# Kernel tuning notes

Hardware: AMD Instinct MI355X
Metric: run time of the kernel (lower is better)

The kernel has to match this reference:

```python
import jax, jax.numpy as jnp
import numpy as np
from jax import lax

T, B, DX, H, DZ = 512, 64, 128, 256, 64
W_SCALE = 0.05


def setup_inputs() -> dict:
    key = jax.random.key(0)
    ks = jax.random.split(key, 16)
    r = lambda k, shape, s=W_SCALE: jax.random.normal(k, shape, dtype=jnp.float32) * s
    return {
        "X": jax.random.normal(ks[0], (T, B, DX), dtype=jnp.float32),
        "Wih_f": r(ks[1], (H, DX)), "Whh_f": r(ks[2], (H, H)),
        "bih_f": r(ks[3], (H,)), "bhh_f": r(ks[4], (H,)),
        "Wih_b": r(ks[5], (H, DX)), "Whh_b": r(ks[6], (H, H)),
        "bih_b": r(ks[7], (H,)), "bhh_b": r(ks[8], (H,)),
        "Wt": r(ks[9], (H, DZ)), "bt": r(ks[10], (H,)),
        "Wmu": r(ks[11], (DZ, H)), "bmu": r(ks[12], (DZ,)),
        "Wsig": r(ks[13], (DZ, H)), "bsig": r(ks[14], (DZ,)),
        "eps": jax.random.normal(ks[15], (T, B, DZ), dtype=jnp.float32),
    }


def _rnn_dir(X, Wih, Whh, bih, bhh):
    # Elman RNN (tanh): h_t = tanh(x_t Wih^T + bih + h_{t-1} Whh^T + bhh)
    xproj = jnp.einsum('tbd,hd->tbh', X, Wih) + bih + bhh  # big GEMM hoisted out of scan

    def step(h, xp):
        h = jnp.tanh(xp + h @ Whh.T)
        return h, h

    h0 = jnp.zeros((X.shape[1], Whh.shape[0]), dtype=X.dtype)
    _, hs = lax.scan(step, h0, xproj)
    return hs  # [T,B,H]


def reference(X, Wih_f, Whh_f, bih_f, bhh_f, Wih_b, Whh_b, bih_b, bhh_b,
              Wt, bt, Wmu, bmu, Wsig, bsig, eps):
    h_left = _rnn_dir(X, Wih_f, Whh_f, bih_f, bhh_f)
    h_right = _rnn_dir(X[::-1], Wih_b, Whh_b, bih_b, bhh_b)[::-1]

    def step(z_prev, inputs):
        hl, hr, eps_t = inputs
        tmp = jnp.tanh(z_prev @ Wt.T + bt)           # transition_net
        h_t = (tmp + hl + hr) * (1.0 / 3.0)
        mu = h_t @ Wmu.T + bmu
        std = jax.nn.softplus(h_t @ Wsig.T + bsig)
        z = mu + std * eps_t                         # reparameterization
        return z, (z, mu, std)

    z0 = jnp.zeros((X.shape[1], Wt.shape[1]), dtype=X.dtype)
    _, (z, mu, std) = lax.scan(step, z0, (h_left, h_right, eps))
    # stack outputs {z_post, mu_post, std_post} into one array [3,T,B,DZ]
    return jnp.stack([z, mu, std])
```

## Files before the change

kernel.cpp:

```cpp
#include <hip/hip_runtime.h>

#define TT 512
#define BB 64
#define DXX 128
#define HH 256
#define DZZ 64

typedef __attribute__((ext_vector_type(8))) short short8;
typedef __attribute__((ext_vector_type(4))) float f32x4;

#define DEV static __device__ __forceinline__
#define MFMA(a,b,c) __builtin_amdgcn_mfma_f32_16x16x32_bf16((a),(b),(c),0,0,0)

DEV unsigned short f2bf(float f){
  unsigned u = __builtin_bit_cast(unsigned, f);
  u += 0x7FFFu + ((u >> 16) & 1u);
  return (unsigned short)(u >> 16);
}
DEV unsigned pack2(float lo, float hi){
  return (unsigned)f2bf(lo) | ((unsigned)f2bf(hi) << 16);
}
DEV float bfLO(unsigned u){ return __builtin_bit_cast(float, u << 16); }
DEV float bfHI(unsigned u){ return __builtin_bit_cast(float, u & 0xffff0000u); }
DEV float ftanh(float x){
  float a = fabsf(x);
  float e = __expf(-2.f * a);
  float r = __builtin_amdgcn_rcpf(1.f + e);
  float t = (1.f - e) * r;
  return copysignf(t, x);
}
DEV float fsoftplus(float x){
  float e = __expf(fminf(x, 20.f));
  float s = __logf(1.f + e);
  return (x > 20.f) ? x : s;
}
DEV void barrier_l(){
  asm volatile("s_waitcnt lgkmcnt(0)\n\ts_barrier" ::: "memory");
}


__global__ __launch_bounds__(256, 2) void phaseA(
    const float* __restrict__ X,
    const float* __restrict__ WihF, const float* __restrict__ bihF, const float* __restrict__ bhhF,
    const float* __restrict__ WihB, const float* __restrict__ bihB, const float* __restrict__ bhhB,
    unsigned short* __restrict__ xpF)
{
  const int bid = blockIdx.x;
  const int d = bid >> 9, s = bid & 511;
  const int ts = d ? (TT - 1 - s) : s;
  const float* W  = d ? WihB : WihF;
  const float* bi = d ? bihB : bihF;
  const float* bh = d ? bhhB : bhhF;

  const int tid = threadIdx.x, q = tid >> 6, l = tid & 63;
  const int l15 = l & 15, l4 = l >> 4;

  short8 wf[4][4];
  f32x4 bias[4];
  #pragma unroll
  for (int ni = 0; ni < 4; ++ni){
    int n = 64*q + 16*ni + l15;
    #pragma unroll
    for (int ks = 0; ks < 4; ++ks){
      const float* p = W + (size_t)n * DXX + ks*32 + l4*8;
      short8 v;
      #pragma unroll
      for (int i = 0; i < 8; ++i) v[i] = (short)f2bf(p[i]);
      wf[ni][ks] = v;
    }
    int n0 = 64*q + 16*ni + 4*l4;
    float4 b1 = *(const float4*)(bi + n0);
    float4 b2 = *(const float4*)(bh + n0);
    bias[ni][0]=b1.x+b2.x; bias[ni][1]=b1.y+b2.y; bias[ni][2]=b1.z+b2.z; bias[ni][3]=b1.w+b2.w;
  }

  #pragma unroll
  for (int bq = 0; bq < 4; ++bq){
    const float* xr = X + ((size_t)ts * 64 + 16*bq + l15) * DXX;
    short8 xf[4];
    #pragma unroll
    for (int ks = 0; ks < 4; ++ks){
      const float* p = xr + ks*32 + l4*8;
      short8 v;
      #pragma unroll
      for (int i = 0; i < 8; ++i) v[i] = (short)f2bf(p[i]);
      xf[ks] = v;
    }

    f32x4 acc[4];
    #pragma unroll
    for (int ni = 0; ni < 4; ++ni) acc[ni] = MFMA(wf[ni][0], xf[0], bias[ni]);
    #pragma unroll
    for (int ks = 1; ks < 4; ++ks)
      #pragma unroll
      for (int ni = 0; ni < 4; ++ni)
        acc[ni] = MFMA(wf[ni][ks], xf[ks], acc[ni]);

    unsigned wd[8];
    #pragma unroll
    for (int ni = 0; ni < 4; ++ni){
      wd[ni*2]   = pack2(acc[ni][0], acc[ni][1]);
      wd[ni*2+1] = pack2(acc[ni][2], acc[ni][3]);
    }
    unsigned short* dst = xpF + ((((size_t)d*TT + s)*4 + bq)*4 + q)*1024 + (size_t)l*16;
    uint4 o0 = {wd[0], wd[1], wd[2], wd[3]};
    uint4 o1 = {wd[4], wd[5], wd[6], wd[7]};
    ((uint4*)dst)[0] = o0;
    ((uint4*)dst)[1] = o1;
  }
}

__global__ __launch_bounds__(256, 1) void phaseB(
    const float* __restrict__ WhhF, const float* __restrict__ WhhB,
    const unsigned short* __restrict__ xpF, unsigned short* __restrict__ hF)
{
  const int dir = blockIdx.x >> 2, bq = blockIdx.x & 3;
  const float* Whh = dir ? WhhB : WhhF;
  const int tid = threadIdx.x, q = tid >> 6, l = tid & 63;
  const int l15 = l & 15, l4 = l >> 4;
  const int swz = (l15 & 7) << 3;
  const int rbase = l15 * 256;

  __shared__ __attribute__((aligned(16))) unsigned short hbuf[2][4096];

  short8 wf[4][8];
  #pragma unroll
  for (int ni = 0; ni < 4; ++ni){
    int n = 64*q + 16*ni + l15;
    #pragma unroll
    for (int ks = 0; ks < 8; ++ks){
      const float* p = Whh + (size_t)n * HH + ks*32 + l4*8;
      short8 v;
      #pragma unroll
      for (int i = 0; i < 8; ++i) v[i] = (short)f2bf(p[i]);
      wf[ni][ks] = v;
    }
  }
  for (int i = tid; i < 2048; i += 256) ((unsigned*)hbuf[0])[i] = 0u;

  const size_t strideS = 16384;
  const size_t laneOff = (size_t)bq*4096 + (size_t)q*1024 + (size_t)l*16;
  const unsigned short* xpP = xpF + (size_t)dir*TT*strideS + laneOff;
  unsigned short* hD = hF + (size_t)dir*TT*strideS + laneOff;

  uint4 xqA0, xqA1, xqB0, xqB1;
  { const uint4* p = (const uint4*)xpP;             xqA0 = p[0]; xqA1 = p[1]; }
  { const uint4* p = (const uint4*)(xpP + strideS); xqB0 = p[0]; xqB1 = p[1]; }

  barrier_l();

  auto bstep = [&](int s, uint4& XQ0, uint4& XQ1,
                   const unsigned short* RD, unsigned short* WR){
    short8 b[8];
    #pragma unroll
    for (int ks = 0; ks < 8; ++ks)
      b[ks] = *(const short8*)(RD + ((rbase + ks*32 + l4*8) ^ swz));
    f32x4 accE[4], accO[4];
    {
      unsigned W8[8] = {XQ0.x, XQ0.y, XQ0.z, XQ0.w, XQ1.x, XQ1.y, XQ1.z, XQ1.w};
      #pragma unroll
      for (int ni = 0; ni < 4; ++ni){
        accE[ni][0] = bfLO(W8[ni*2]);   accE[ni][1] = bfHI(W8[ni*2]);
        accE[ni][2] = bfLO(W8[ni*2+1]); accE[ni][3] = bfHI(W8[ni*2+1]);
        accO[ni][0] = 0.f; accO[ni][1] = 0.f; accO[ni][2] = 0.f; accO[ni][3] = 0.f;
      }
    }
    {
      int sn = (s + 2 < TT) ? s + 2 : TT - 1;
      const uint4* src = (const uint4*)(xpP + (size_t)sn * strideS);
      XQ0 = src[0]; XQ1 = src[1];
    }
    #pragma unroll
    for (int ks = 0; ks < 8; ks += 2){
      #pragma unroll
      for (int ni = 0; ni < 4; ++ni){
        accE[ni] = MFMA(wf[ni][ks],   b[ks],   accE[ni]);
        accO[ni] = MFMA(wf[ni][ks+1], b[ks+1], accO[ni]);
      }
    }
    unsigned wd[8];
    #pragma unroll
    for (int ni = 0; ni < 4; ++ni){
      float t0 = ftanh(accE[ni][0] + accO[ni][0]);
      float t1 = ftanh(accE[ni][1] + accO[ni][1]);
      float t2 = ftanh(accE[ni][2] + accO[ni][2]);
      float t3 = ftanh(accE[ni][3] + accO[ni][3]);
      unsigned lo = pack2(t0, t1), hi = pack2(t2, t3);
      wd[ni*2] = lo; wd[ni*2+1] = hi;
      int ea = rbase + ((64*q + 16*ni + 4*l4) ^ swz);
      uint2 v; v.x = lo; v.y = hi;
      *(uint2*)(WR + ea) = v;
    }
    {
      size_t off = (size_t)(dir ? (TT - 1 - s) : s) * strideS;
      uint4 o0 = {wd[0], wd[1], wd[2], wd[3]};
      uint4 o1 = {wd[4], wd[5], wd[6], wd[7]};
      *(uint4*)(hD + off)     = o0;
      *(uint4*)(hD + off + 8) = o1;
    }
    barrier_l();
  };

  for (int s = 0; s < TT; s += 2){
    bstep(s,     xqA0, xqA1, hbuf[0], hbuf[1]);
    bstep(s + 1, xqB0, xqB1, hbuf[1], hbuf[0]);
  }
}

__global__ __launch_bounds__(256, 1) void phaseC(
    const float* __restrict__ Wt,  const float* __restrict__ bt,
    const float* __restrict__ Wmu, const float* __restrict__ bmu,
    const float* __restrict__ Wsig,const float* __restrict__ bsig,
    const float* __restrict__ eps, const unsigned short* __restrict__ hF,
    float* __restrict__ out)
{
  const int bq = blockIdx.x;
  const int tid = threadIdx.x, q = tid >> 6, l = tid & 63;
  const int l15 = l & 15, l4 = l >> 4;
  const int swz = (l15 & 7) << 3;
  const int rbase = l15 * 256;
  const int zrbase = l15 * 64;

  __shared__ __attribute__((aligned(16))) unsigned short zbuf[1024];
  __shared__ __attribute__((aligned(16))) unsigned short hbuf[4096];

  short8 wtf[4][2]; f32x4 btb[4];
  #pragma unroll
  for (int ni = 0; ni < 4; ++ni){
    int n = 64*q + 16*ni + l15;
    #pragma unroll
    for (int ks = 0; ks < 2; ++ks){
      const float* p = Wt + (size_t)n * DZZ + ks*32 + l4*8;
      short8 v;
      #pragma unroll
      for (int i = 0; i < 8; ++i) v[i] = (short)f2bf(p[i]);
      wtf[ni][ks] = v;
    }
    float4 b4 = *(const float4*)(bt + 64*q + 16*ni + 4*l4);
    btb[ni][0]=b4.x; btb[ni][1]=b4.y; btb[ni][2]=b4.z; btb[ni][3]=b4.w;
  }
  short8 wm[8], wsg[8];
  {
    int r = 16*q + l15;
    #pragma unroll
    for (int ks = 0; ks < 8; ++ks){
      const float* pm = Wmu  + (size_t)r * HH + ks*32 + l4*8;
      const float* ps = Wsig + (size_t)r * HH + ks*32 + l4*8;
      short8 vm, vs;
      #pragma unroll
      for (int i = 0; i < 8; ++i){ vm[i] = (short)f2bf(pm[i]); vs[i] = (short)f2bf(ps[i]); }
      wm[ks] = vm; wsg[ks] = vs;
    }
  }
  f32x4 bm4, bs4;
  {
    float4 a = *(const float4*)(bmu  + 16*q + 4*l4);
    float4 b = *(const float4*)(bsig + 16*q + 4*l4);
    bm4[0]=a.x; bm4[1]=a.y; bm4[2]=a.z; bm4[3]=a.w;
    bs4[0]=b.x; bs4[1]=b.y; bs4[2]=b.z; bs4[3]=b.w;
  }
  for (int i = tid; i < 512; i += 256) ((unsigned*)zbuf)[i] = 0u;

  const size_t strideS = 16384;
  const size_t laneOff = (size_t)bq*4096 + (size_t)q*1024 + (size_t)l*16;
  const unsigned short* hLp = hF + laneOff;
  const unsigned short* hRp = hLp + (size_t)TT * strideS;
  const float* eP = eps + ((size_t)(16*bq + l15)) * 64 + 16*q + 4*l4;

  uint4 hlA0, hlA1, hrA0, hrA1, hlB0, hlB1, hrB0, hrB1;
  f32x4 efA, efB;
  {
    const uint4* sl = (const uint4*)hLp;              hlA0 = sl[0]; hlA1 = sl[1];
    const uint4* sr = (const uint4*)hRp;              hrA0 = sr[0]; hrA1 = sr[1];
    const uint4* tl = (const uint4*)(hLp + strideS);  hlB0 = tl[0]; hlB1 = tl[1];
    const uint4* tr = (const uint4*)(hRp + strideS);  hrB0 = tr[0]; hrB1 = tr[1];
    float4 e0 = *(const float4*)eP;
    float4 e1 = *(const float4*)(eP + 4096);
    efA[0]=e0.x; efA[1]=e0.y; efA[2]=e0.z; efA[3]=e0.w;
    efB[0]=e1.x; efB[1]=e1.y; efB[2]=e1.z; efB[3]=e1.w;
  }
  const size_t TBZ = (size_t)TT * 64 * 64;
  const f32x4 zero4 = {0.f, 0.f, 0.f, 0.f};
  barrier_l();

  auto cstep = [&](int t, uint4& HL0, uint4& HL1, uint4& HR0, uint4& HR1, f32x4& EF){
    short8 zb0 = *(const short8*)(zbuf + ((zrbase +  0 + l4*8) ^ swz));
    short8 zb1 = *(const short8*)(zbuf + ((zrbase + 32 + l4*8) ^ swz));
    f32x4 at[4];
    #pragma unroll
    for (int ni = 0; ni < 4; ++ni) at[ni] = MFMA(wtf[ni][0], zb0, btb[ni]);
    #pragma unroll
    for (int ni = 0; ni < 4; ++ni) at[ni] = MFMA(wtf[ni][1], zb1, at[ni]);
    {
      unsigned HLw[8] = {HL0.x, HL0.y, HL0.z, HL0.w, HL1.x, HL1.y, HL1.z, HL1.w};
      unsigned HRw[8] = {HR0.x, HR0.y, HR0.z, HR0.w, HR1.x, HR1.y, HR1.z, HR1.w};
      #pragma unroll
      for (int ni = 0; ni < 4; ++ni){
        unsigned wl0 = HLw[ni*2], wl1 = HLw[ni*2+1];
        unsigned wr0 = HRw[ni*2], wr1 = HRw[ni*2+1];
        float h0 = (ftanh(at[ni][0]) + bfLO(wl0) + bfLO(wr0)) * (1.f/3.f);
        float h1 = (ftanh(at[ni][1]) + bfHI(wl0) + bfHI(wr0)) * (1.f/3.f);
        float h2 = (ftanh(at[ni][2]) + bfLO(wl1) + bfLO(wr1)) * (1.f/3.f);
        float h3 = (ftanh(at[ni][3]) + bfHI(wl1) + bfHI(wr1)) * (1.f/3.f);
        int ea = rbase + ((64*q + 16*ni + 4*l4) ^ swz);
        uint2 v; v.x = pack2(h0, h1); v.y = pack2(h2, h3);
        *(uint2*)(hbuf + ea) = v;
      }
    }
    {
      int tn = (t + 2 < TT) ? t + 2 : TT - 1;
      const uint4* sl = (const uint4*)(hLp + (size_t)tn*strideS);
      const uint4* sr = (const uint4*)(hRp + (size_t)tn*strideS);
      HL0 = sl[0]; HL1 = sl[1]; HR0 = sr[0]; HR1 = sr[1];
    }
    barrier_l();

    short8 hb[8];
    #pragma unroll
    for (int ks = 0; ks < 8; ++ks)
      hb[ks] = *(const short8*)(hbuf + ((rbase + ks*32 + l4*8) ^ swz));
    f32x4 am0 = MFMA(wm[0],  hb[0], bm4);
    f32x4 as0 = MFMA(wsg[0], hb[0], bs4);
    f32x4 am1 = MFMA(wm[4],  hb[4], zero4);
    f32x4 as1 = MFMA(wsg[4], hb[4], zero4);
    #pragma unroll
    for (int ks = 1; ks < 4; ++ks){
      am0 = MFMA(wm[ks],    hb[ks],   am0);
      as0 = MFMA(wsg[ks],   hb[ks],   as0);
      am1 = MFMA(wm[ks+4],  hb[ks+4], am1);
      as1 = MFMA(wsg[ks+4], hb[ks+4], as1);
    }
    f32x4 mu = am0 + am1;
    f32x4 sg = as0 + as1;
    f32x4 dz, dsp;
    #pragma unroll
    for (int reg = 0; reg < 4; ++reg){
      float sp = fsoftplus(sg[reg]);
      dz[reg] = __builtin_fmaf(sp, EF[reg], mu[reg]);
      dsp[reg] = sp;
    }
    {
      int zea = zrbase + ((16*q + 4*l4) ^ swz);
      uint2 v; v.x = pack2(dz[0], dz[1]); v.y = pack2(dz[2], dz[3]);
      *(uint2*)(zbuf + zea) = v;
    }
    {
      int tn = (t + 2 < TT) ? t + 2 : TT - 1;
      float4 e4 = *(const float4*)(eP + (size_t)tn*4096);
      EF[0]=e4.x; EF[1]=e4.y; EF[2]=e4.z; EF[3]=e4.w;
    }
    {
      size_t ob = ((size_t)t*64 + 16*bq + l15)*64 + 16*q + 4*l4;
      *(float4*)(out + ob)         = *(float4*)&dz;
      *(float4*)(out + TBZ + ob)   = *(float4*)&mu;
      *(float4*)(out + 2*TBZ + ob) = *(float4*)&dsp;
    }
    barrier_l();
  };

  for (int t = 0; t < TT; t += 2){
    cstep(t,     hlA0, hlA1, hrA0, hrA1, efA);
    cstep(t + 1, hlB0, hlB1, hrB0, hrB1, efB);
  }
}

extern "C" void kernel_launch(void* const* d_in, const int* in_sizes, int n_in,
                              void* d_out, int out_size, void* d_ws, size_t ws_size,
                              hipStream_t stream)
{
  const float* X      = (const float*)d_in[0];
  const float* Wih_f  = (const float*)d_in[1];
  const float* Whh_f  = (const float*)d_in[2];
  const float* bih_f  = (const float*)d_in[3];
  const float* bhh_f  = (const float*)d_in[4];
  const float* Wih_b  = (const float*)d_in[5];
  const float* Whh_b  = (const float*)d_in[6];
  const float* bih_b  = (const float*)d_in[7];
  const float* bhh_b  = (const float*)d_in[8];
  const float* Wt     = (const float*)d_in[9];
  const float* bt     = (const float*)d_in[10];
  const float* Wmu    = (const float*)d_in[11];
  const float* bmu    = (const float*)d_in[12];
  const float* Wsig   = (const float*)d_in[13];
  const float* bsig   = (const float*)d_in[14];
  const float* eps    = (const float*)d_in[15];

  unsigned short* xpF = (unsigned short*)d_ws;
  unsigned short* hF  = xpF + (size_t)2 * TT * 16384;

  phaseA<<<dim3(1024), dim3(256), 0, stream>>>(X, Wih_f, bih_f, bhh_f, Wih_b, bih_b, bhh_b, xpF);
  phaseB<<<dim3(8), dim3(256), 0, stream>>>(Whh_f, Whh_b, xpF, hF);
  phaseC<<<dim3(4), dim3(256), 0, stream>>>(Wt, bt, Wmu, bmu, Wsig, bsig, eps, hF, (float*)d_out);
}
```

Baseline: 1.132 ms.

## Hoist hl+hr projections out of latent scan and halve recurrence block width

The latent scan's mu/sigma projections are linear in h_t, so the hl+hr contribution is precomputed for all timesteps in a new fully parallel kernel and written to workspace. The sequential scan then only multiplies the tanh(transition) term by Wmu/Wsig, with the 1/3 factor folded into the weights. Both sequential kernels now use two waves per block instead of four, each wave owning twice as many output columns. This is meant to cut barrier cost and per-step latency on the serial critical path. The trade-offs are an extra kernel launch, extra workspace traffic, and more register pressure per wave.

```diff
diff --git a/kernel.cpp b/kernel.cpp
--- a/kernel.cpp
+++ b/kernel.cpp
@@ -1,7 +1,6 @@
 #include <hip/hip_runtime.h>
 
 #define TT 512
-#define BB 64
 #define DXX 128
 #define HH 256
 #define DZZ 64
@@ -86,7 +85,6 @@
       for (int i = 0; i < 8; ++i) v[i] = (short)f2bf(p[i]);
       xf[ks] = v;
     }
-
     f32x4 acc[4];
     #pragma unroll
     for (int ni = 0; ni < 4; ++ni) acc[ni] = MFMA(wf[ni][0], xf[0], bias[ni]);
@@ -110,135 +108,127 @@
   }
 }
 
-__global__ __launch_bounds__(256, 1) void phaseB(
+__global__ __launch_bounds__(128, 1) void phaseB(
     const float* __restrict__ WhhF, const float* __restrict__ WhhB,
     const unsigned short* __restrict__ xpF, unsigned short* __restrict__ hF)
 {
   const int dir = blockIdx.x >> 2, bq = blockIdx.x & 3;
   const float* Whh = dir ? WhhB : WhhF;
+  const int tid = threadIdx.x, qc = tid >> 6, l = tid & 63;
+  const int l15 = l & 15, l4 = l >> 4;
+  const int swz = (l15 & 7) << 3;
+  const int rbase = l15 * 256;
+
+  __shared__ __attribute__((aligned(16))) unsigned short hbuf[2][4096];
+
+  short8 wf[8][8];
+  #pragma unroll
+  for (int ni = 0; ni < 8; ++ni){
+    int n = 128*qc + 16*ni + l15;
+    #pragma unroll
+    for (int ks = 0; ks < 8; ++ks){
+      const float* p = Whh + (size_t)n * HH + ks*32 + l4*8;
+      short8 v;
+      #pragma unroll
+      for (int i = 0; i < 8; ++i) v[i] = (short)f2bf(p[i]);
+      wf[ni][ks] = v;
+    }
+  }
+  for (int i = tid; i < 2048; i += 128) ((unsigned*)hbuf[0])[i] = 0u;
+
+  const size_t strideS = 16384;
+  const size_t base = (size_t)dir*TT*strideS + (size_t)bq*4096 + (size_t)l*16;
+  const unsigned short* xpP = xpF + base;
+  unsigned short* hD = hF + base;
+
+  uint4 xA[4], xB[4];
+  #pragma unroll
+  for (int hi = 0; hi < 2; ++hi)
+    #pragma unroll
+    for (int pt = 0; pt < 2; ++pt){
+      xA[hi*2+pt] = *(const uint4*)(xpP + (size_t)(2*qc+hi)*1024 + pt*8);
+      xB[hi*2+pt] = *(const uint4*)(xpP + strideS + (size_t)(2*qc+hi)*1024 + pt*8);
+    }
+  barrier_l();
+
+  auto bstep = [&](int s, uint4 (&X)[4]){
+    f32x4 acc[8];
+    #pragma unroll
+    for (int ni = 0; ni < 8; ++ni){
+      int hi = ni >> 2, no = ni & 3;
+      uint4 u = X[hi*2 + (no >> 1)];
+      unsigned w0 = (no & 1) ? u.z : u.x;
+      unsigned w1 = (no & 1) ? u.w : u.y;
+      acc[ni][0] = bfLO(w0); acc[ni][1] = bfHI(w0);
+      acc[ni][2] = bfLO(w1); acc[ni][3] = bfHI(w1);
+    }
+    {
+      int sn = (s + 2 < TT) ? s + 2 : TT - 1;
+      #pragma unroll
+      for (int hi = 0; hi < 2; ++hi)
+        #pragma unroll
+        for (int pt = 0; pt < 2; ++pt)
+          X[hi*2+pt] = *(const uint4*)(xpP + (size_t)sn*strideS + (size_t)(2*qc+hi)*1024 + pt*8);
+    }
+    const unsigned short* RD = hbuf[s & 1];
+    unsigned short* WR = hbuf[(s & 1) ^ 1];
+    #pragma unroll
+    for (int ksc = 0; ksc < 8; ksc += 4){
+      short8 b[4];
+      #pragma unroll
+      for (int k2 = 0; k2 < 4; ++k2)
+        b[k2] = *(const short8*)(RD + ((rbase + (ksc+k2)*32 + l4*8) ^ swz));
+      #pragma unroll
+      for (int k2 = 0; k2 < 4; ++k2)
+        #pragma unroll
+        for (int ni = 0; ni < 8; ++ni)
+          acc[ni] = MFMA(wf[ni][ksc+k2], b[k2], acc[ni]);
+    }
+    unsigned wd[16];
+    #pragma unroll
+    for (int ni = 0; ni < 8; ++ni){
+      float t0 = ftanh(acc[ni][0]), t1 = ftanh(acc[ni][1]);
+      float t2 = ftanh(acc[ni][2]), t3 = ftanh(acc[ni][3]);
+      unsigned lo = pack2(t0, t1), hi2 = pack2(t2, t3);
+      wd[ni*2] = lo; wd[ni*2+1] = hi2;
+      int ea = rbase + ((128*qc + 16*ni + 4*l4) ^ swz);
+      uint2 v; v.x = lo; v.y = hi2;
+      *(uint2*)(WR + ea) = v;
+    }
+    {
+      size_t off = (size_t)(dir ? (TT - 1 - s) : s) * strideS;
+      #pragma unroll
+      for (int hi = 0; hi < 2; ++hi){
+        unsigned short* dst = hD + off + (size_t)(2*qc+hi)*1024;
+        uint4 o0 = {wd[hi*8+0], wd[hi*8+1], wd[hi*8+2], wd[hi*8+3]};
+        uint4 o1 = {wd[hi*8+4], wd[hi*8+5], wd[hi*8+6], wd[hi*8+7]};
+        *(uint4*)dst       = o0;
+        *(uint4*)(dst + 8) = o1;
+      }
+    }
+    barrier_l();
+  };
+
+  for (int s = 0; s < TT; s += 2){
+    bstep(s,     xA);
+    bstep(s + 1, xB);
+  }
+}
+
+__global__ __launch_bounds__(256, 2) void phaseP(
+    const float* __restrict__ Wmu, const float* __restrict__ bmu,
+    const float* __restrict__ Wsig,const float* __restrict__ bsig,
+    const unsigned short* __restrict__ hF, float* __restrict__ MS)
+{
+  const int bid = blockIdx.x;
+  const int t = bid >> 2, bq = bid & 3;
   const int tid = threadIdx.x, q = tid >> 6, l = tid & 63;
   const int l15 = l & 15, l4 = l >> 4;
   const int swz = (l15 & 7) << 3;
   const int rbase = l15 * 256;
 
-  __shared__ __attribute__((aligned(16))) unsigned short hbuf[2][4096];
-
-  short8 wf[4][8];
-  #pragma unroll
-  for (int ni = 0; ni < 4; ++ni){
-    int n = 64*q + 16*ni + l15;
-    #pragma unroll
-    for (int ks = 0; ks < 8; ++ks){
-      const float* p = Whh + (size_t)n * HH + ks*32 + l4*8;
-      short8 v;
-      #pragma unroll
-      for (int i = 0; i < 8; ++i) v[i] = (short)f2bf(p[i]);
-      wf[ni][ks] = v;
-    }
-  }
-  for (int i = tid; i < 2048; i += 256) ((unsigned*)hbuf[0])[i] = 0u;
-
-  const size_t strideS = 16384;
-  const size_t laneOff = (size_t)bq*4096 + (size_t)q*1024 + (size_t)l*16;
-  const unsigned short* xpP = xpF + (size_t)dir*TT*strideS + laneOff;
-  unsigned short* hD = hF + (size_t)dir*TT*strideS + laneOff;
-
-  uint4 xqA0, xqA1, xqB0, xqB1;
-  { const uint4* p = (const uint4*)xpP;             xqA0 = p[0]; xqA1 = p[1]; }
-  { const uint4* p = (const uint4*)(xpP + strideS); xqB0 = p[0]; xqB1 = p[1]; }
-
-  barrier_l();
-
-  auto bstep = [&](int s, uint4& XQ0, uint4& XQ1,
-                   const unsigned short* RD, unsigned short* WR){
-    short8 b[8];
-    #pragma unroll
-    for (int ks = 0; ks < 8; ++ks)
-      b[ks] = *(const short8*)(RD + ((rbase + ks*32 + l4*8) ^ swz));
-    f32x4 accE[4], accO[4];
-    {
-      unsigned W8[8] = {XQ0.x, XQ0.y, XQ0.z, XQ0.w, XQ1.x, XQ1.y, XQ1.z, XQ1.w};
-      #pragma unroll
-      for (int ni = 0; ni < 4; ++ni){
-        accE[ni][0] = bfLO(W8[ni*2]);   accE[ni][1] = bfHI(W8[ni*2]);
-        accE[ni][2] = bfLO(W8[ni*2+1]); accE[ni][3] = bfHI(W8[ni*2+1]);
-        accO[ni][0] = 0.f; accO[ni][1] = 0.f; accO[ni][2] = 0.f; accO[ni][3] = 0.f;
-      }
-    }
-    {
-      int sn = (s + 2 < TT) ? s + 2 : TT - 1;
-      const uint4* src = (const uint4*)(xpP + (size_t)sn * strideS);
-      XQ0 = src[0]; XQ1 = src[1];
-    }
-    #pragma unroll
-    for (int ks = 0; ks < 8; ks += 2){
-      #pragma unroll
-      for (int ni = 0; ni < 4; ++ni){
-        accE[ni] = MFMA(wf[ni][ks],   b[ks],   accE[ni]);
-        accO[ni] = MFMA(wf[ni][ks+1], b[ks+1], accO[ni]);
-      }
-    }
-    unsigned wd[8];
-    #pragma unroll
-    for (int ni = 0; ni < 4; ++ni){
-      float t0 = ftanh(accE[ni][0] + accO[ni][0]);
-      float t1 = ftanh(accE[ni][1] + accO[ni][1]);
-      float t2 = ftanh(accE[ni][2] + accO[ni][2]);
-      float t3 = ftanh(accE[ni][3] + accO[ni][3]);
-      unsigned lo = pack2(t0, t1), hi = pack2(t2, t3);
-      wd[ni*2] = lo; wd[ni*2+1] = hi;
-      int ea = rbase + ((64*q + 16*ni + 4*l4) ^ swz);
-      uint2 v; v.x = lo; v.y = hi;
-      *(uint2*)(WR + ea) = v;
-    }
-    {
-      size_t off = (size_t)(dir ? (TT - 1 - s) : s) * strideS;
-      uint4 o0 = {wd[0], wd[1], wd[2], wd[3]};
-      uint4 o1 = {wd[4], wd[5], wd[6], wd[7]};
-      *(uint4*)(hD + off)     = o0;
-      *(uint4*)(hD + off + 8) = o1;
-    }
-    barrier_l();
-  };
-
-  for (int s = 0; s < TT; s += 2){
-    bstep(s,     xqA0, xqA1, hbuf[0], hbuf[1]);
-    bstep(s + 1, xqB0, xqB1, hbuf[1], hbuf[0]);
-  }
-}
-
-__global__ __launch_bounds__(256, 1) void phaseC(
-    const float* __restrict__ Wt,  const float* __restrict__ bt,
-    const float* __restrict__ Wmu, const float* __restrict__ bmu,
-    const float* __restrict__ Wsig,const float* __restrict__ bsig,
-    const float* __restrict__ eps, const unsigned short* __restrict__ hF,
-    float* __restrict__ out)
-{
-  const int bq = blockIdx.x;
-  const int tid = threadIdx.x, q = tid >> 6, l = tid & 63;
-  const int l15 = l & 15, l4 = l >> 4;
-  const int swz = (l15 & 7) << 3;
-  const int rbase = l15 * 256;
-  const int zrbase = l15 * 64;
-
-  __shared__ __attribute__((aligned(16))) unsigned short zbuf[1024];
   __shared__ __attribute__((aligned(16))) unsigned short hbuf[4096];
 
-  short8 wtf[4][2]; f32x4 btb[4];
-  #pragma unroll
-  for (int ni = 0; ni < 4; ++ni){
-    int n = 64*q + 16*ni + l15;
-    #pragma unroll
-    for (int ks = 0; ks < 2; ++ks){
-      const float* p = Wt + (size_t)n * DZZ + ks*32 + l4*8;
-      short8 v;
-      #pragma unroll
-      for (int i = 0; i < 8; ++i) v[i] = (short)f2bf(p[i]);
-      wtf[ni][ks] = v;
-    }
-    float4 b4 = *(const float4*)(bt + 64*q + 16*ni + 4*l4);
-    btb[ni][0]=b4.x; btb[ni][1]=b4.y; btb[ni][2]=b4.z; btb[ni][3]=b4.w;
-  }
   short8 wm[8], wsg[8];
   {
     int r = 16*q + l15;
@@ -248,7 +238,10 @@
       const float* ps = Wsig + (size_t)r * HH + ks*32 + l4*8;
       short8 vm, vs;
       #pragma unroll
-      for (int i = 0; i < 8; ++i){ vm[i] = (short)f2bf(pm[i]); vs[i] = (short)f2bf(ps[i]); }
+      for (int i = 0; i < 8; ++i){
+        vm[i] = (short)f2bf(pm[i] * (1.f/3.f));
+        vs[i] = (short)f2bf(ps[i] * (1.f/3.f));
+      }
       wm[ks] = vm; wsg[ks] = vs;
     }
   }
@@ -259,108 +252,198 @@
     bm4[0]=a.x; bm4[1]=a.y; bm4[2]=a.z; bm4[3]=a.w;
     bs4[0]=b.x; bs4[1]=b.y; bs4[2]=b.z; bs4[3]=b.w;
   }
-  for (int i = tid; i < 512; i += 256) ((unsigned*)zbuf)[i] = 0u;
 
   const size_t strideS = 16384;
   const size_t laneOff = (size_t)bq*4096 + (size_t)q*1024 + (size_t)l*16;
-  const unsigned short* hLp = hF + laneOff;
-  const unsigned short* hRp = hLp + (size_t)TT * strideS;
-  const float* eP = eps + ((size_t)(16*bq + l15)) * 64 + 16*q + 4*l4;
-
-  uint4 hlA0, hlA1, hrA0, hrA1, hlB0, hlB1, hrB0, hrB1;
-  f32x4 efA, efB;
+  const unsigned short* hl = hF + (size_t)t*strideS + laneOff;
+  const unsigned short* hr = hl + (size_t)TT*strideS;
   {
-    const uint4* sl = (const uint4*)hLp;              hlA0 = sl[0]; hlA1 = sl[1];
-    const uint4* sr = (const uint4*)hRp;              hrA0 = sr[0]; hrA1 = sr[1];
-    const uint4* tl = (const uint4*)(hLp + strideS);  hlB0 = tl[0]; hlB1 = tl[1];
-    const uint4* tr = (const uint4*)(hRp + strideS);  hrB0 = tr[0]; hrB1 = tr[1];
-    float4 e0 = *(const float4*)eP;
-    float4 e1 = *(const float4*)(eP + 4096);
-    efA[0]=e0.x; efA[1]=e0.y; efA[2]=e0.z; efA[3]=e0.w;
-    efB[0]=e1.x; efB[1]=e1.y; efB[2]=e1.z; efB[3]=e1.w;
-  }
+    uint4 a0 = ((const uint4*)hl)[0], a1 = ((const uint4*)hl)[1];
+    uint4 b0 = ((const uint4*)hr)[0], b1 = ((const uint4*)hr)[1];
+    unsigned HL[8] = {a0.x,a0.y,a0.z,a0.w,a1.x,a1.y,a1.z,a1.w};
+    unsigned HR[8] = {b0.x,b0.y,b0.z,b0.w,b1.x,b1.y,b1.z,b1.w};
+    #pragma unroll
+    for (int ni = 0; ni < 4; ++ni){
+      float h0 = bfLO(HL[ni*2])   + bfLO(HR[ni*2]);
+      float h1 = bfHI(HL[ni*2])   + bfHI(HR[ni*2]);
+      float h2 = bfLO(HL[ni*2+1]) + bfLO(HR[ni*2+1]);
+      float h3 = bfHI(HL[ni*2+1]) + bfHI(HR[ni*2+1]);
+      int ea = rbase + ((64*q + 16*ni + 4*l4) ^ swz);
+      uint2 v; v.x = pack2(h0, h1); v.y = pack2(h2, h3);
+      *(uint2*)(hbuf + ea) = v;
+    }
+  }
+  __syncthreads();
+
+  short8 hb[8];
+  #pragma unroll
+  for (int ks = 0; ks < 8; ++ks)
+    hb[ks] = *(const short8*)(hbuf + ((rbase + ks*32 + l4*8) ^ swz));
+  const f32x4 zero4 = {0.f,0.f,0.f,0.f};
+  f32x4 am0 = MFMA(wm[0],  hb[0], bm4);
+  f32x4 as0 = MFMA(wsg[0], hb[0], bs4);
+  f32x4 am1 = MFMA(wm[4],  hb[4], zero4);
+  f32x4 as1 = MFMA(wsg[4], hb[4], zero4);
+  #pragma unroll
+  for (int ks = 1; ks < 4; ++ks){
+    am0 = MFMA(wm[ks],    hb[ks],   am0);
+    as0 = MFMA(wsg[ks],   hb[ks],   as0);
+    am1 = MFMA(wm[ks+4],  hb[ks+4], am1);
+    as1 = MFMA(wsg[ks+4], hb[ks+4], as1);
+  }
+  f32x4 mu = am0 + am1;
+  f32x4 sg = as0 + as1;
+  float* dst = MS + ((((size_t)t*4 + bq)*4 + q)*64 + (size_t)l)*8;
+  *(float4*)dst       = *(float4*)&mu;
+  *(float4*)(dst + 4) = *(float4*)&sg;
+}
+
+__global__ __launch_bounds__(128, 1) void phaseC(
+    const float* __restrict__ Wt,  const float* __restrict__ bt,
+    const float* __restrict__ Wmu, const float* __restrict__ Wsig,
+    const float* __restrict__ eps, const float* __restrict__ MS,
+    float* __restrict__ out)
+{
+  const int bq = blockIdx.x;
+  const int tid = threadIdx.x, qc = tid >> 6, l = tid & 63;
+  const int l15 = l & 15, l4 = l >> 4;
+  const int swz = (l15 & 7) << 3;
+  const int rbase = l15 * 256;
+  const int zrbase = l15 * 64;
+
+  __shared__ __attribute__((aligned(16))) unsigned short zbuf[1024];
+  __shared__ __attribute__((aligned(16))) unsigned short ubuf[4096];
+
+  short8 wtf[8][2]; f32x4 btb[8];
+  #pragma unroll
+  for (int ni = 0; ni < 8; ++ni){
+    int n = 128*qc + 16*ni + l15;
+    #pragma unroll
+    for (int ks = 0; ks < 2; ++ks){
+      const float* p = Wt + (size_t)n * DZZ + ks*32 + l4*8;
+      short8 v;
+      #pragma unroll
+      for (int i = 0; i < 8; ++i) v[i] = (short)f2bf(p[i]);
+      wtf[ni][ks] = v;
+    }
+    float4 b4 = *(const float4*)(bt + 128*qc + 16*ni + 4*l4);
+    btb[ni][0]=b4.x; btb[ni][1]=b4.y; btb[ni][2]=b4.z; btb[ni][3]=b4.w;
+  }
+  short8 wm[2][8], wsg[2][8];
+  #pragma unroll
+  for (int nj = 0; nj < 2; ++nj){
+    int r = 32*qc + 16*nj + l15;
+    #pragma unroll
+    for (int ks = 0; ks < 8; ++ks){
+      const float* pm = Wmu  + (size_t)r * HH + ks*32 + l4*8;
+      const float* ps = Wsig + (size_t)r * HH + ks*32 + l4*8;
+      short8 vm, vs;
+      #pragma unroll
+      for (int i = 0; i < 8; ++i){
+        vm[i] = (short)f2bf(pm[i] * (1.f/3.f));
+        vs[i] = (short)f2bf(ps[i] * (1.f/3.f));
+      }
+      wm[nj][ks] = vm; wsg[nj][ks] = vs;
+    }
+  }
+  for (int i = tid; i < 512; i += 128) ((unsigned*)zbuf)[i] = 0u;
+
+  const float* msP = MS + (((size_t)bq*4 + 2*qc)*64 + (size_t)l)*8;
+  const float* eP  = eps + ((size_t)(16*bq + l15))*64 + 32*qc + 4*l4;
   const size_t TBZ = (size_t)TT * 64 * 64;
-  const f32x4 zero4 = {0.f, 0.f, 0.f, 0.f};
+
+  f32x4 MPa[2], SPa[2], EFa[2], MPb[2], SPb[2], EFb[2];
+  #pragma unroll
+  for (int nj = 0; nj < 2; ++nj){
+    float4 m0 = *(const float4*)(msP + nj*512);
+    float4 s0 = *(const float4*)(msP + nj*512 + 4);
+    float4 m1 = *(const float4*)(msP + 8192 + nj*512);
+    float4 s1 = *(const float4*)(msP + 8192 + nj*512 + 4);
+    float4 e0 = *(const float4*)(eP + nj*16);
+    float4 e1 = *(const float4*)(eP + 4096 + nj*16);
+    MPa[nj][0]=m0.x;MPa[nj][1]=m0.y;MPa[nj][2]=m0.z;MPa[nj][3]=m0.w;
+    SPa[nj][0]=s0.x;SPa[nj][1]=s0.y;SPa[nj][2]=s0.z;SPa[nj][3]=s0.w;
+    MPb[nj][0]=m1.x;MPb[nj][1]=m1.y;MPb[nj][2]=m1.z;MPb[nj][3]=m1.w;
+    SPb[nj][0]=s1.x;SPb[nj][1]=s1.y;SPb[nj][2]=s1.z;SPb[nj][3]=s1.w;
+    EFa[nj][0]=e0.x;EFa[nj][1]=e0.y;EFa[nj][2]=e0.z;EFa[nj][3]=e0.w;
+    EFb[nj][0]=e1.x;EFb[nj][1]=e1.y;EFb[nj][2]=e1.z;EFb[nj][3]=e1.w;
+  }
   barrier_l();
 
-  auto cstep = [&](int t, uint4& HL0, uint4& HL1, uint4& HR0, uint4& HR1, f32x4& EF){
+  auto cstep = [&](int t, f32x4 (&MP)[2], f32x4 (&SP)[2], f32x4 (&EF)[2]){
     short8 zb0 = *(const short8*)(zbuf + ((zrbase +  0 + l4*8) ^ swz));
     short8 zb1 = *(const short8*)(zbuf + ((zrbase + 32 + l4*8) ^ swz));
-    f32x4 at[4];
-    #pragma unroll
-    for (int ni = 0; ni < 4; ++ni) at[ni] = MFMA(wtf[ni][0], zb0, btb[ni]);
-    #pragma unroll
-    for (int ni = 0; ni < 4; ++ni) at[ni] = MFMA(wtf[ni][1], zb1, at[ni]);
-    {
-      unsigned HLw[8] = {HL0.x, HL0.y, HL0.z, HL0.w, HL1.x, HL1.y, HL1.z, HL1.w};
-      unsigned HRw[8] = {HR0.x, HR0.y, HR0.z, HR0.w, HR1.x, HR1.y, HR1.z, HR1.w};
-      #pragma unroll
-      for (int ni = 0; ni < 4; ++ni){
-        unsigned wl0 = HLw[ni*2], wl1 = HLw[ni*2+1];
-        unsigned wr0 = HRw[ni*2], wr1 = HRw[ni*2+1];
-        float h0 = (ftanh(at[ni][0]) + bfLO(wl0) + bfLO(wr0)) * (1.f/3.f);
-        float h1 = (ftanh(at[ni][1]) + bfHI(wl0) + bfHI(wr0)) * (1.f/3.f);
-        float h2 = (ftanh(at[ni][2]) + bfLO(wl1) + bfLO(wr1)) * (1.f/3.f);
-        float h3 = (ftanh(at[ni][3]) + bfHI(wl1) + bfHI(wr1)) * (1.f/3.f);
-        int ea = rbase + ((64*q + 16*ni + 4*l4) ^ swz);
-        uint2 v; v.x = pack2(h0, h1); v.y = pack2(h2, h3);
-        *(uint2*)(hbuf + ea) = v;
-      }
-    }
+    f32x4 at[8];
+    #pragma unroll
+    for (int ni = 0; ni < 8; ++ni) at[ni] = MFMA(wtf[ni][0], zb0, btb[ni]);
+    #pragma unroll
+    for (int ni = 0; ni < 8; ++ni) at[ni] = MFMA(wtf[ni][1], zb1, at[ni]);
+    #pragma unroll
+    for (int ni = 0; ni < 8; ++ni){
+      float u0 = ftanh(at[ni][0]), u1 = ftanh(at[ni][1]);
+      float u2 = ftanh(at[ni][2]), u3 = ftanh(at[ni][3]);
+      int ea = rbase + ((128*qc + 16*ni + 4*l4) ^ swz);
+      uint2 v; v.x = pack2(u0, u1); v.y = pack2(u2, u3);
+      *(uint2*)(ubuf + ea) = v;
+    }
+    barrier_l();
+
+    f32x4 am[2], as2[2];
+    #pragma unroll
+    for (int ksc = 0; ksc < 8; ksc += 4){
+      short8 hb[4];
+      #pragma unroll
+      for (int k2 = 0; k2 < 4; ++k2)
+        hb[k2] = *(const short8*)(ubuf + ((rbase + (ksc+k2)*32 + l4*8) ^ swz));
+      if (ksc == 0){
+        #pragma unroll
+        for (int nj = 0; nj < 2; ++nj){ am[nj] = MP[nj]; as2[nj] = SP[nj]; }
+      }
+      #pragma unroll
+      for (int k2 = 0; k2 < 4; ++k2)
+        #pragma unroll
+        for (int nj = 0; nj < 2; ++nj){
+          am[nj]  = MFMA(wm[nj][ksc+k2],  hb[k2], am[nj]);
+          as2[nj] = MFMA(wsg[nj][ksc+k2], hb[k2], as2[nj]);
+        }
+    }
+    f32x4 dz[2], dsp[2];
+    #pragma unroll
+    for (int nj = 0; nj < 2; ++nj)
+      #pragma unroll
+      for (int reg = 0; reg < 4; ++reg){
+        float sp = fsoftplus(as2[nj][reg]);
+        dz[nj][reg]  = __builtin_fmaf(sp, EF[nj][reg], am[nj][reg]);
+        dsp[nj][reg] = sp;
+      }
     {
       int tn = (t + 2 < TT) ? t + 2 : TT - 1;
-      const uint4* sl = (const uint4*)(hLp + (size_t)tn*strideS);
-      const uint4* sr = (const uint4*)(hRp + (size_t)tn*strideS);
-      HL0 = sl[0]; HL1 = sl[1]; HR0 = sr[0]; HR1 = sr[1];
-    }
-    barrier_l();
-
-    short8 hb[8];
-    #pragma unroll
-    for (int ks = 0; ks < 8; ++ks)
-      hb[ks] = *(const short8*)(hbuf + ((rbase + ks*32 + l4*8) ^ swz));
-    f32x4 am0 = MFMA(wm[0],  hb[0], bm4);
-    f32x4 as0 = MFMA(wsg[0], hb[0], bs4);
-    f32x4 am1 = MFMA(wm[4],  hb[4], zero4);
-    f32x4 as1 = MFMA(wsg[4], hb[4], zero4);
-    #pragma unroll
-    for (int ks = 1; ks < 4; ++ks){
-      am0 = MFMA(wm[ks],    hb[ks],   am0);
-      as0 = MFMA(wsg[ks],   hb[ks],   as0);
-      am1 = MFMA(wm[ks+4],  hb[ks+4], am1);
-      as1 = MFMA(wsg[ks+4], hb[ks+4], as1);
-    }
-    f32x4 mu = am0 + am1;
-    f32x4 sg = as0 + as1;
-    f32x4 dz, dsp;
-    #pragma unroll
-    for (int reg = 0; reg < 4; ++reg){
-      float sp = fsoftplus(sg[reg]);
-      dz[reg] = __builtin_fmaf(sp, EF[reg], mu[reg]);
-      dsp[reg] = sp;
-    }
-    {
-      int zea = zrbase + ((16*q + 4*l4) ^ swz);
-      uint2 v; v.x = pack2(dz[0], dz[1]); v.y = pack2(dz[2], dz[3]);
+      #pragma unroll
+      for (int nj = 0; nj < 2; ++nj){
+        float4 m = *(const float4*)(msP + (size_t)tn*8192 + nj*512);
+        float4 s = *(const float4*)(msP + (size_t)tn*8192 + nj*512 + 4);
+        float4 e = *(const float4*)(eP + (size_t)tn*4096 + nj*16);
+        MP[nj][0]=m.x;MP[nj][1]=m.y;MP[nj][2]=m.z;MP[nj][3]=m.w;
+        SP[nj][0]=s.x;SP[nj][1]=s.y;SP[nj][2]=s.z;SP[nj][3]=s.w;
+        EF[nj][0]=e.x;EF[nj][1]=e.y;EF[nj][2]=e.z;EF[nj][3]=e.w;
+      }
+    }
+    #pragma unroll
+    for (int nj = 0; nj < 2; ++nj){
+      int zea = zrbase + ((32*qc + 16*nj + 4*l4) ^ swz);
+      uint2 v; v.x = pack2(dz[nj][0], dz[nj][1]); v.y = pack2(dz[nj][2], dz[nj][3]);
       *(uint2*)(zbuf + zea) = v;
-    }
-    {
-      int tn = (t + 2 < TT) ? t + 2 : TT - 1;
-      float4 e4 = *(const float4*)(eP + (size_t)tn*4096);
-      EF[0]=e4.x; EF[1]=e4.y; EF[2]=e4.z; EF[3]=e4.w;
-    }
-    {
-      size_t ob = ((size_t)t*64 + 16*bq + l15)*64 + 16*q + 4*l4;
-      *(float4*)(out + ob)         = *(float4*)&dz;
-      *(float4*)(out + TBZ + ob)   = *(float4*)&mu;
-      *(float4*)(out + 2*TBZ + ob) = *(float4*)&dsp;
+      size_t ob = ((size_t)t*64 + 16*bq + l15)*64 + 32*qc + 16*nj + 4*l4;
+      *(float4*)(out + ob)         = *(float4*)&dz[nj];
+      *(float4*)(out + TBZ + ob)   = *(float4*)&am[nj];
+      *(float4*)(out + 2*TBZ + ob) = *(float4*)&dsp[nj];
     }
     barrier_l();
   };
 
   for (int t = 0; t < TT; t += 2){
-    cstep(t,     hlA0, hlA1, hrA0, hrA1, efA);
-    cstep(t + 1, hlB0, hlB1, hrB0, hrB1, efB);
+    cstep(t,     MPa, SPa, EFa);
+    cstep(t + 1, MPb, SPb, EFb);
   }
 }
 
@@ -387,8 +470,10 @@
 
   unsigned short* xpF = (unsigned short*)d_ws;
   unsigned short* hF  = xpF + (size_t)2 * TT * 16384;
+  float* MS = (float*)d_ws;
 
   phaseA<<<dim3(1024), dim3(256), 0, stream>>>(X, Wih_f, bih_f, bhh_f, Wih_b, bih_b, bhh_b, xpF);
-  phaseB<<<dim3(8), dim3(256), 0, stream>>>(Whh_f, Whh_b, xpF, hF);
-  phaseC<<<dim3(4), dim3(256), 0, stream>>>(Wt, bt, Wmu, bmu, Wsig, bsig, eps, hF, (float*)d_out);
-}
+  phaseB<<<dim3(8), dim3(128), 0, stream>>>(Whh_f, Whh_b, xpF, hF);
+  phaseP<<<dim3(2048), dim3(256), 0, stream>>>(Wmu, bmu, Wsig, bsig, hF, MS);
+  phaseC<<<dim3(4), dim3(128), 0, stream>>>(Wt, bt, Wmu, Wsig, eps, MS, (float*)d_out);
+}
```

New measurement: 1.964 ms. +73.5%, slower.
